# Kernel optimization log

Measured on AMD Instinct MI355X. Metric: run time of the kernel, lower is better.

## Reference

```python
import jax, jax.numpy as jnp
import numpy as np

B, C, VC, H, W = 4, 256, 128, 64, 64


def setup_inputs() -> dict:
    key = jax.random.key(0)
    kx, kq, kk, kv = jax.random.split(key, 4)
    # Conv2d 1x1 no-bias weights are just [out_channels, in_channels] matrices.
    s = 1.0 / np.sqrt(C)
    return {
        "x": jax.random.normal(kx, (B, C, H, W), dtype=jnp.float32),
        "Wq": jax.random.uniform(kq, (VC, C), minval=-s, maxval=s, dtype=jnp.float32),
        "Wk": jax.random.uniform(kk, (VC, C), minval=-s, maxval=s, dtype=jnp.float32),
        "Wv": jax.random.uniform(kv, (VC, C), minval=-s, maxval=s, dtype=jnp.float32),
    }


def reference(x, Wq, Wk, Wv):
    # 1x1 convs == per-pixel channel GEMMs
    Q = jnp.einsum('bchw,dc->bdhw', x, Wq)  # [B, VC, H, W]
    K = jnp.einsum('bchw,dc->bdhw', x, Wk)
    V = jnp.einsum('bchw,dc->bdhw', x, Wv)
    b, d, h, w = Q.shape
    # affinity over all spatial pairs: [B, H, W, H, W]
    aff = jnp.einsum('bdij,bdkl->bijkl', Q, K).reshape(b, h, w, h * w)
    aff = jax.nn.softmax(aff, axis=3).reshape(b, h, w, h, w)
    # attention-weighted aggregation of values
    out = jnp.einsum('bijkl,bdkl->bdij', aff, V)  # [B, VC, H, W]
    return out
```

## Files before the change

kernel.cpp:

```cpp
#include <hip/hip_runtime.h>
#include <hip/hip_bf16.h>

#define B_ 4
#define C_ 256
#define D_ 128
#define N_ 4096

typedef float f32x4 __attribute__((ext_vector_type(4)));
typedef short bf16x8 __attribute__((ext_vector_type(8)));
typedef short s16x4 __attribute__((ext_vector_type(4)));
typedef unsigned short u16;
typedef unsigned int u32;

__device__ __forceinline__ u16 f2bf(float f) {
  unsigned u = __float_as_uint(f);
  u += 0x7fffu + ((u >> 16) & 1u);
  return (u16)(u >> 16);
}
__device__ __forceinline__ float bf2f(u16 v) {
  return __uint_as_float(((u32)v) << 16);
}
__device__ __forceinline__ u32 cvt_pk_bf16(float a, float b) {
  u32 r;
  asm("v_cvt_pk_bf16_f32 %0, %1, %2" : "=v"(r) : "v"(a), "v"(b));
  return r;
}

__global__ __launch_bounds__(256) void castw_kernel(
    const float* __restrict__ Wq, const float* __restrict__ Wk,
    const float* __restrict__ Wv, u16* __restrict__ Whi,
    u16* __restrict__ Wlo) {
  const int i = blockIdx.x * 256 + threadIdx.x;
  const int m = i >> 13;
  const int j = (i & 8191) * 4;
  const float* src = (m == 0) ? Wq : (m == 1) ? Wk : Wv;
  const float scale = (m == 0) ? 1.44269504f : 1.0f;
  const float4 v = *(const float4*)(src + j);
  const float vv[4] = {v.x * scale, v.y * scale, v.z * scale, v.w * scale};
  s16x4 h, l;
#pragma unroll
  for (int k = 0; k < 4; ++k) {
    const u16 hb = f2bf(vv[k]);
    h[k] = (short)hb;
    l[k] = (short)f2bf(vv[k] - bf2f(hb));
  }
  *(s16x4*)&Whi[m * 32768 + j] = h;
  *(s16x4*)&Wlo[m * 32768 + j] = l;
}

__global__ __launch_bounds__(256, 2) void proj_kernel(
    const float* __restrict__ x, const u16* __restrict__ Whi,
    const u16* __restrict__ Wlo, u16* __restrict__ Qo, u16* __restrict__ Ko,
    u16* __restrict__ Vt) {
  __shared__ __align__(16) u16 xs_h[32 * 256];
  __shared__ __align__(16) u16 xs_l[32 * 256];

  const int n0 = blockIdx.x * 32;
  const int b = blockIdx.y;
  const int t = threadIdx.x;
  const int w = t >> 6, lane = t & 63, g = lane >> 4, c = lane & 15;

  {
    const float* xb = x + ((size_t)b * C_) * N_ + n0;
#pragma unroll
    for (int r = 0; r < 8; ++r) {
      const int id = r * 256 + t;
      const int cr = id >> 3, nq = (id & 7) * 4;
      const float4 v = *(const float4*)(xb + (size_t)cr * N_ + nq);
      const float vv[4] = {v.x, v.y, v.z, v.w};
#pragma unroll
      for (int k2 = 0; k2 < 4; ++k2) {
        const int idx2 = (nq + k2) * 256 + (cr ^ (((nq + k2) & 7) << 3));
        const u16 hb = f2bf(vv[k2]);
        xs_h[idx2] = hb;
        xs_l[idx2] = f2bf(vv[k2] - bf2f(hb));
      }
    }
  }
  __syncthreads();

  if (w < 2) {
    const size_t wo = (size_t)w * 32768;
    u16* __restrict__ O = (w == 0 ? Qo : Ko) + (size_t)b * N_ * D_;
#pragma unroll 1
    for (int dt = 0; dt < 8; ++dt) {
      bf16x8 wfh[8], wfl[8];
#pragma unroll
      for (int kc = 0; kc < 8; ++kc) {
        const size_t off = wo + (size_t)(dt * 16 + c) * 256 + kc * 32 + g * 8;
        wfh[kc] = *(const bf16x8*)&Whi[off];
        wfl[kc] = *(const bf16x8*)&Wlo[off];
      }
#pragma unroll
      for (int nt = 0; nt < 2; ++nt) {
        f32x4 a = {0.f, 0.f, 0.f, 0.f};
#pragma unroll
        for (int kc = 0; kc < 8; ++kc) {
          const int xi = (nt * 16 + c) * 256 +
                         ((kc * 32 + g * 8) ^ ((c & 7) << 3));
          const bf16x8 xh = *(const bf16x8*)&xs_h[xi];
          const bf16x8 xl = *(const bf16x8*)&xs_l[xi];
          a = __builtin_amdgcn_mfma_f32_16x16x32_bf16(xh, wfh[kc], a, 0, 0, 0);
          a = __builtin_amdgcn_mfma_f32_16x16x32_bf16(xh, wfl[kc], a, 0, 0, 0);
          a = __builtin_amdgcn_mfma_f32_16x16x32_bf16(xl, wfh[kc], a, 0, 0, 0);
        }
#pragma unroll
        for (int i = 0; i < 4; ++i)
          O[(size_t)(n0 + nt * 16 + g * 4 + i) * D_ + dt * 16 + c] = f2bf(a[i]);
      }
    }
  } else {
    const size_t wo = (size_t)2 * 32768;
    const int d0 = (w - 2) * 64;
    u16* __restrict__ O = Vt + (size_t)b * D_ * N_;
#pragma unroll 1
    for (int dt = 0; dt < 4; ++dt) {
      bf16x8 wfh[8], wfl[8];
#pragma unroll
      for (int kc = 0; kc < 8; ++kc) {
        const size_t off =
            wo + (size_t)(d0 + dt * 16 + c) * 256 + kc * 32 + g * 8;
        wfh[kc] = *(const bf16x8*)&Whi[off];
        wfl[kc] = *(const bf16x8*)&Wlo[off];
      }
#pragma unroll
      for (int nt = 0; nt < 2; ++nt) {
        f32x4 a = {0.f, 0.f, 0.f, 0.f};
#pragma unroll
        for (int kc = 0; kc < 8; ++kc) {
          const int xi = (nt * 16 + c) * 256 +
                         ((kc * 32 + g * 8) ^ ((c & 7) << 3));
          const bf16x8 xh = *(const bf16x8*)&xs_h[xi];
          const bf16x8 xl = *(const bf16x8*)&xs_l[xi];
          a = __builtin_amdgcn_mfma_f32_16x16x32_bf16(wfh[kc], xh, a, 0, 0, 0);
          a = __builtin_amdgcn_mfma_f32_16x16x32_bf16(wfl[kc], xh, a, 0, 0, 0);
          a = __builtin_amdgcn_mfma_f32_16x16x32_bf16(wfh[kc], xl, a, 0, 0, 0);
        }
#pragma unroll
        for (int i = 0; i < 4; ++i)
          O[(size_t)(d0 + dt * 16 + g * 4 + i) * N_ + n0 + nt * 16 + c] =
              f2bf(a[i]);
      }
    }
  }
}

__device__ __forceinline__ int kIdx(int row, int col) {
  return row * 128 + (col ^ ((row & 7) << 3));
}
__device__ __forceinline__ int vIdx(int d, int col) {
  return d * 64 + (col ^ ((d & 7) << 3));
}
__device__ __forceinline__ int kprm(int q) {
  const int ct = q >> 2, qq = q & 3;
  return ((ct >> 1) << 5) +
         (((qq >> 1) == (ct & 1)) ? (qq << 3) : (((qq ^ 2) << 3) + 4));
}

__global__ __launch_bounds__(256, 2) void attn_kernel(
    const u16* __restrict__ Q, const u16* __restrict__ K,
    const u16* __restrict__ Vt, u16* __restrict__ op,
    float* __restrict__ mb, float* __restrict__ lb,
    float* __restrict__ outf, int qt, int rem) {
  __shared__ __align__(16) u16 lds_k[64 * 128];
  __shared__ __align__(16) u16 lds_vt[128 * 64];

  const int b = blockIdx.y;
  const int sid = blockIdx.z;
  const int q0 = blockIdx.x * 128;
  const int NT = qt + (sid < rem ? 1 : 0);
  const int t0 = sid * qt + (sid < rem ? sid : rem);
  const int k0 = t0 * 64;
  const int t = threadIdx.x;
  const int w = t >> 6, lane = t & 63, g = lane >> 4, c = lane & 15;
  const int qw = q0 + w * 32;
  const bool ghi = (g & 2) != 0;

  const u16* __restrict__ Qb = Q + (size_t)b * N_ * D_;
  const u16* __restrict__ Kb = K + (size_t)b * N_ * D_;
  const u16* __restrict__ Vb = Vt + (size_t)b * D_ * N_;

  bf16x8 qf[2][4];
#pragma unroll
  for (int qh = 0; qh < 2; ++qh)
#pragma unroll
    for (int kc = 0; kc < 4; ++kc)
      qf[qh][kc] =
          *(const bf16x8*)&Qb[(size_t)(qw + qh * 16 + c) * D_ + kc * 32 + g * 8];

  f32x4 acc[8][2];
#pragma unroll
  for (int dt = 0; dt < 8; ++dt)
#pragma unroll
    for (int qh = 0; qh < 2; ++qh) acc[dt][qh] = (f32x4){0.f, 0.f, 0.f, 0.f};
  float mrow[2] = {-3.0e38f, -3.0e38f};
  float lrow[2] = {0.f, 0.f};
  const float THR = 11.5415603f;

  bf16x8 krg[4], vrg[4];
  auto load_tile = [&](int kbase) {
#pragma unroll
    for (int i = 0; i < 4; ++i) {
      const int idx = i * 256 + t;
      krg[i] = *(const bf16x8*)&Kb[(size_t)(kbase + (idx >> 4)) * D_ + (idx & 15) * 8];
      vrg[i] = *(const bf16x8*)&Vb[(size_t)(idx >> 3) * N_ + kbase + (idx & 7) * 8];
    }
  };
  load_tile(k0);

  for (int kt = 0; kt < NT; ++kt) {
    __syncthreads();
#pragma unroll
    for (int i = 0; i < 4; ++i) {
      const int idx = i * 256 + t;
      *(bf16x8*)&lds_k[kIdx(idx >> 4, (idx & 15) * 8)] = krg[i];
      const int d = idx >> 3, rc = idx & 7;
      s16x4 lo, hi;
      lo[0] = vrg[i][0]; lo[1] = vrg[i][1]; lo[2] = vrg[i][2]; lo[3] = vrg[i][3];
      hi[0] = vrg[i][4]; hi[1] = vrg[i][5]; hi[2] = vrg[i][6]; hi[3] = vrg[i][7];
      *(s16x4*)&lds_vt[vIdx(d, kprm(rc * 2))] = lo;
      *(s16x4*)&lds_vt[vIdx(d, kprm(rc * 2 + 1))] = hi;
    }
    if (kt + 1 < NT) load_tile(k0 + (kt + 1) * 64);
    __syncthreads();

    f32x4 s[4][2];
#pragma unroll
    for (int ct = 0; ct < 4; ++ct)
#pragma unroll
      for (int qh = 0; qh < 2; ++qh) s[ct][qh] = (f32x4){0.f, 0.f, 0.f, 0.f};
    __builtin_amdgcn_s_setprio(1);
#pragma unroll
    for (int kc = 0; kc < 4; ++kc) {
#pragma unroll
      for (int ct = 0; ct < 4; ++ct) {
        const bf16x8 kf =
            *(const bf16x8*)&lds_k[kIdx(ct * 16 + c, kc * 32 + g * 8)];
        s[ct][0] = __builtin_amdgcn_mfma_f32_16x16x32_bf16(kf, qf[0][kc], s[ct][0], 0, 0, 0);
        s[ct][1] = __builtin_amdgcn_mfma_f32_16x16x32_bf16(kf, qf[1][kc], s[ct][1], 0, 0, 0);
      }
    }
    __builtin_amdgcn_s_setprio(0);

    float pm[2];
#pragma unroll
    for (int qh = 0; qh < 2; ++qh) {
      const float m0 = fmaxf(fmaxf(s[0][qh][0], s[0][qh][1]),
                             fmaxf(s[0][qh][2], s[0][qh][3]));
      const float m1 = fmaxf(fmaxf(s[1][qh][0], s[1][qh][1]),
                             fmaxf(s[1][qh][2], s[1][qh][3]));
      const float m2 = fmaxf(fmaxf(s[2][qh][0], s[2][qh][1]),
                             fmaxf(s[2][qh][2], s[2][qh][3]));
      const float m3 = fmaxf(fmaxf(s[3][qh][0], s[3][qh][1]),
                             fmaxf(s[3][qh][2], s[3][qh][3]));
      float p = fmaxf(fmaxf(m0, m1), fmaxf(m2, m3));
      p = fmaxf(p, __shfl_xor(p, 16));
      p = fmaxf(p, __shfl_xor(p, 32));
      pm[qh] = p;
    }
    const bool need =
        __any((pm[0] > mrow[0] + THR) || (pm[1] > mrow[1] + THR));
    if (need) {
#pragma unroll
      for (int qh = 0; qh < 2; ++qh) {
        const float mnew = fmaxf(mrow[qh], pm[qh]);
        const float scl = exp2f(mrow[qh] - mnew);
        lrow[qh] *= scl;
        mrow[qh] = mnew;
#pragma unroll
        for (int dt = 0; dt < 8; ++dt) {
          acc[dt][qh][0] *= scl; acc[dt][qh][1] *= scl;
          acc[dt][qh][2] *= scl; acc[dt][qh][3] *= scl;
        }
      }
    }
#pragma unroll
    for (int qh = 0; qh < 2; ++qh) {
      float rs = 0.f;
#pragma unroll
      for (int ct = 0; ct < 4; ++ct)
#pragma unroll
        for (int i = 0; i < 4; ++i) {
          const float p = exp2f(s[ct][qh][i] - mrow[qh]);
          s[ct][qh][i] = p;
          rs += p;
        }
      rs += __shfl_xor(rs, 16);
      rs += __shfl_xor(rs, 32);
      lrow[qh] += rs;
    }

    u32 pfw[2][2][4];
#pragma unroll
    for (int kc = 0; kc < 2; ++kc) {
#pragma unroll
      for (int qh = 0; qh < 2; ++qh) {
        const u32 lo0 = cvt_pk_bf16(s[kc * 2][qh][0], s[kc * 2][qh][1]);
        const u32 lo1 = cvt_pk_bf16(s[kc * 2][qh][2], s[kc * 2][qh][3]);
        const u32 hi0 = cvt_pk_bf16(s[kc * 2 + 1][qh][0], s[kc * 2 + 1][qh][1]);
        const u32 hi1 = cvt_pk_bf16(s[kc * 2 + 1][qh][2], s[kc * 2 + 1][qh][3]);
        pfw[kc][qh][0] = ghi ? hi0 : lo0;
        pfw[kc][qh][1] = ghi ? hi1 : lo1;
        const u32 s0 = ghi ? lo0 : hi0;
        const u32 s1 = ghi ? lo1 : hi1;
        pfw[kc][qh][2] = (u32)__shfl_xor((int)s0, 32);
        pfw[kc][qh][3] = (u32)__shfl_xor((int)s1, 32);
      }
    }

#pragma unroll
    for (int kc = 0; kc < 2; ++kc) {
      union { u32 w[4]; bf16x8 v; } u0, u1;
#pragma unroll
      for (int j = 0; j < 4; ++j) { u0.w[j] = pfw[kc][0][j]; u1.w[j] = pfw[kc][1][j]; }
      __builtin_amdgcn_s_setprio(1);
#pragma unroll
      for (int dt = 0; dt < 8; ++dt) {
        const bf16x8 vf =
            *(const bf16x8*)&lds_vt[vIdx(dt * 16 + c, kc * 32 + g * 8)];
        acc[dt][0] = __builtin_amdgcn_mfma_f32_16x16x32_bf16(vf, u0.v, acc[dt][0], 0, 0, 0);
        acc[dt][1] = __builtin_amdgcn_mfma_f32_16x16x32_bf16(vf, u1.v, acc[dt][1], 0, 0, 0);
      }
      __builtin_amdgcn_s_setprio(0);
    }
  }

#pragma unroll
  for (int qh = 0; qh < 2; ++qh) {
    const int n = qw + qh * 16 + c;
    if (mb) {
      u16* __restrict__ ob = op + ((size_t)(sid * B_ + b) * D_) * N_;
#pragma unroll
      for (int dt = 0; dt < 8; ++dt)
#pragma unroll
        for (int i = 0; i < 4; ++i)
          ob[(size_t)(dt * 16 + g * 4 + i) * N_ + n] = f2bf(acc[dt][qh][i]);
      if (g == 0) {
        mb[(size_t)(sid * B_ + b) * N_ + n] = mrow[qh];
        lb[(size_t)(sid * B_ + b) * N_ + n] = lrow[qh];
      }
    } else {
      const float linv = 1.0f / lrow[qh];
      float* __restrict__ ob = outf + (size_t)b * D_ * N_;
#pragma unroll
      for (int dt = 0; dt < 8; ++dt)
#pragma unroll
        for (int i = 0; i < 4; ++i)
          ob[(size_t)(dt * 16 + g * 4 + i) * N_ + n] = acc[dt][qh][i] * linv;
    }
  }
}

__global__ __launch_bounds__(256) void combine_kernel(
    const u16* __restrict__ op, const float* __restrict__ mbu,
    const float* __restrict__ lbu, float* __restrict__ out, int S) {
  const int idx = blockIdx.x * 256 + threadIdx.x;
  const int n0 = (idx & (N_ / 4 - 1)) * 4;
  const int bd = idx >> 10;
  const int b = bd >> 7, d = bd & (D_ - 1);

  float4 msv[8], lsv[8];
  float M0 = -3e38f, M1 = -3e38f, M2 = -3e38f, M3 = -3e38f;
#pragma unroll
  for (int s = 0; s < 8; ++s)
    if (s < S) {
      msv[s] = *(const float4*)&mbu[(size_t)(s * B_ + b) * N_ + n0];
      lsv[s] = *(const float4*)&lbu[(size_t)(s * B_ + b) * N_ + n0];
      M0 = fmaxf(M0, msv[s].x); M1 = fmaxf(M1, msv[s].y);
      M2 = fmaxf(M2, msv[s].z); M3 = fmaxf(M3, msv[s].w);
    }
  float d0 = 0.f, d1 = 0.f, d2 = 0.f, d3 = 0.f;
  float a0 = 0.f, a1 = 0.f, a2 = 0.f, a3 = 0.f;
#pragma unroll
  for (int s = 0; s < 8; ++s)
    if (s < S) {
      const float w0 = exp2f(msv[s].x - M0);
      const float w1 = exp2f(msv[s].y - M1);
      const float w2 = exp2f(msv[s].z - M2);
      const float w3 = exp2f(msv[s].w - M3);
      d0 += lsv[s].x * w0; d1 += lsv[s].y * w1;
      d2 += lsv[s].z * w2; d3 += lsv[s].w * w3;
      const s16x4 o =
          *(const s16x4*)&op[((size_t)(s * B_ + b) * D_ + d) * N_ + n0];
      a0 += w0 * bf2f((u16)o[0]); a1 += w1 * bf2f((u16)o[1]);
      a2 += w2 * bf2f((u16)o[2]); a3 += w3 * bf2f((u16)o[3]);
    }
  float4 r = {a0 / d0, a1 / d1, a2 / d2, a3 / d3};
  *(float4*)&out[((size_t)b * D_ + d) * N_ + n0] = r;
}

extern "C" void kernel_launch(void* const* d_in, const int* in_sizes, int n_in,
                              void* d_out, int out_size, void* d_ws, size_t ws_size,
                              hipStream_t stream) {
  const float* x  = (const float*)d_in[0];
  const float* Wq = (const float*)d_in[1];
  const float* Wk = (const float*)d_in[2];
  const float* Wv = (const float*)d_in[3];
  float* out = (float*)d_out;

  u16* whi  = (u16*)d_ws;
  u16* wlo  = whi + (size_t)3 * 128 * 256;
  u16* q_ws = wlo + (size_t)3 * 128 * 256;
  u16* k_ws = q_ws + (size_t)B_ * N_ * D_;
  u16* v_ws = k_ws + (size_t)B_ * N_ * D_;

  castw_kernel<<<96, 256, 0, stream>>>(Wq, Wk, Wv, whi, wlo);
  proj_kernel<<<dim3(N_ / 32, B_), 256, 0, stream>>>(x, whi, wlo, q_ws, k_ws,
                                                     v_ws);

  const size_t baseB =
      ((size_t)6 * 128 * 256 + (size_t)3 * B_ * N_ * D_) * 2;
  int S = 0;
  const int cands[4] = {6, 4, 2, 1};
  for (int ci = 0; ci < 4; ++ci) {
    const int cand = cands[ci];
    const size_t need = baseB + (size_t)cand * ((size_t)B_ * D_ * N_ * 2 +
                                                (size_t)2 * B_ * N_ * 4);
    if (ws_size >= need) { S = cand; break; }
  }
  if (S > 1) {
    u16* opb = (u16*)((char*)d_ws + baseB);
    float* mbuf = (float*)(opb + (size_t)S * B_ * D_ * N_);
    float* lbuf = mbuf + (size_t)S * B_ * N_;
    attn_kernel<<<dim3(N_ / 128, B_, S), 256, 0, stream>>>(
        q_ws, k_ws, v_ws, opb, mbuf, lbuf, nullptr, 64 / S, 64 % S);
    combine_kernel<<<(B_ * D_ * N_ / 4) / 256, 256, 0, stream>>>(opb, mbuf,
                                                                 lbuf, out, S);
  } else {
    attn_kernel<<<dim3(N_ / 128, B_, 1), 256, 0, stream>>>(
        q_ws, k_ws, v_ws, nullptr, nullptr, nullptr, out, 64, 0);
  }
}
```

Baseline: 103.2 us.

## Compute softmax row sums via MFMA with ones and enlarge projection tiles

The attention kernel no longer reduces softmax row sums with per-lane adds and cross-lane shuffles. It accumulates them with an extra MFMA against a ones vector, using the same bf16-rounded probabilities that feed the PV product. The running-max shuffle reduction now runs only inside the rare rescale branch, and the threshold test uses per-lane partial maxima. The projection kernel moves to 512-thread blocks covering 64 pixels, so each weight-fragment load serves more pixel tiles, at the cost of doubled LDS per block.

```diff
diff --git a/kernel.cpp b/kernel.cpp
--- a/kernel.cpp
+++ b/kernel.cpp
@@ -48,14 +48,14 @@
   *(s16x4*)&Wlo[m * 32768 + j] = l;
 }
 
-__global__ __launch_bounds__(256, 2) void proj_kernel(
+__global__ __launch_bounds__(512, 2) void proj_kernel(
     const float* __restrict__ x, const u16* __restrict__ Whi,
     const u16* __restrict__ Wlo, u16* __restrict__ Qo, u16* __restrict__ Ko,
     u16* __restrict__ Vt) {
-  __shared__ __align__(16) u16 xs_h[32 * 256];
-  __shared__ __align__(16) u16 xs_l[32 * 256];
-
-  const int n0 = blockIdx.x * 32;
+  __shared__ __align__(16) u16 xs_h[64 * 256];
+  __shared__ __align__(16) u16 xs_l[64 * 256];
+
+  const int n0 = blockIdx.x * 64;
   const int b = blockIdx.y;
   const int t = threadIdx.x;
   const int w = t >> 6, lane = t & 63, g = lane >> 4, c = lane & 15;
@@ -64,8 +64,8 @@
     const float* xb = x + ((size_t)b * C_) * N_ + n0;
 #pragma unroll
     for (int r = 0; r < 8; ++r) {
-      const int id = r * 256 + t;
-      const int cr = id >> 3, nq = (id & 7) * 4;
+      const int id = r * 512 + t;
+      const int cr = id >> 4, nq = (id & 15) * 4;
       const float4 v = *(const float4*)(xb + (size_t)cr * N_ + nq);
       const float vv[4] = {v.x, v.y, v.z, v.w};
 #pragma unroll
@@ -79,11 +79,14 @@
   }
   __syncthreads();
 
-  if (w < 2) {
-    const size_t wo = (size_t)w * 32768;
-    u16* __restrict__ O = (w == 0 ? Qo : Ko) + (size_t)b * N_ * D_;
+  if (w < 4) {
+    const int m = w >> 1;
+    const size_t wo = (size_t)m * 32768;
+    const int dtb = (w & 1) * 4;
+    u16* __restrict__ O = (m == 0 ? Qo : Ko) + (size_t)b * N_ * D_;
 #pragma unroll 1
-    for (int dt = 0; dt < 8; ++dt) {
+    for (int dti = 0; dti < 4; ++dti) {
+      const int dt = dtb + dti;
       bf16x8 wfh[8], wfl[8];
 #pragma unroll
       for (int kc = 0; kc < 8; ++kc) {
@@ -92,7 +95,7 @@
         wfl[kc] = *(const bf16x8*)&Wlo[off];
       }
 #pragma unroll
-      for (int nt = 0; nt < 2; ++nt) {
+      for (int nt = 0; nt < 4; ++nt) {
         f32x4 a = {0.f, 0.f, 0.f, 0.f};
 #pragma unroll
         for (int kc = 0; kc < 8; ++kc) {
@@ -111,20 +114,20 @@
     }
   } else {
     const size_t wo = (size_t)2 * 32768;
-    const int d0 = (w - 2) * 64;
+    const int dtb = (w - 4) * 2;
     u16* __restrict__ O = Vt + (size_t)b * D_ * N_;
 #pragma unroll 1
-    for (int dt = 0; dt < 4; ++dt) {
+    for (int dti = 0; dti < 2; ++dti) {
+      const int dt = dtb + dti;
       bf16x8 wfh[8], wfl[8];
 #pragma unroll
       for (int kc = 0; kc < 8; ++kc) {
-        const size_t off =
-            wo + (size_t)(d0 + dt * 16 + c) * 256 + kc * 32 + g * 8;
+        const size_t off = wo + (size_t)(dt * 16 + c) * 256 + kc * 32 + g * 8;
         wfh[kc] = *(const bf16x8*)&Whi[off];
         wfl[kc] = *(const bf16x8*)&Wlo[off];
       }
 #pragma unroll
-      for (int nt = 0; nt < 2; ++nt) {
+      for (int nt = 0; nt < 4; ++nt) {
         f32x4 a = {0.f, 0.f, 0.f, 0.f};
 #pragma unroll
         for (int kc = 0; kc < 8; ++kc) {
@@ -138,8 +141,7 @@
         }
 #pragma unroll
         for (int i = 0; i < 4; ++i)
-          O[(size_t)(d0 + dt * 16 + g * 4 + i) * N_ + n0 + nt * 16 + c] =
-              f2bf(a[i]);
+          O[(size_t)(dt * 16 + g * 4 + i) * N_ + n0 + nt * 16 + c] = f2bf(a[i]);
       }
     }
   }
@@ -189,13 +191,19 @@
           *(const bf16x8*)&Qb[(size_t)(qw + qh * 16 + c) * D_ + kc * 32 + g * 8];
 
   f32x4 acc[8][2];
+  f32x4 accl[2];
 #pragma unroll
   for (int dt = 0; dt < 8; ++dt)
 #pragma unroll
     for (int qh = 0; qh < 2; ++qh) acc[dt][qh] = (f32x4){0.f, 0.f, 0.f, 0.f};
+  accl[0] = (f32x4){0.f, 0.f, 0.f, 0.f};
+  accl[1] = (f32x4){0.f, 0.f, 0.f, 0.f};
   float mrow[2] = {-3.0e38f, -3.0e38f};
-  float lrow[2] = {0.f, 0.f};
   const float THR = 11.5415603f;
+
+  bf16x8 onesv;
+#pragma unroll
+  for (int j = 0; j < 8; ++j) onesv[j] = (short)0x3F80;
 
   bf16x8 krg[4], vrg[4];
   auto load_tile = [&](int kbase) {
@@ -242,7 +250,7 @@
     }
     __builtin_amdgcn_s_setprio(0);
 
-    float pm[2];
+    float pml[2];
 #pragma unroll
     for (int qh = 0; qh < 2; ++qh) {
       const float m0 = fmaxf(fmaxf(s[0][qh][0], s[0][qh][1]),
@@ -253,20 +261,21 @@
                              fmaxf(s[2][qh][2], s[2][qh][3]));
       const float m3 = fmaxf(fmaxf(s[3][qh][0], s[3][qh][1]),
                              fmaxf(s[3][qh][2], s[3][qh][3]));
-      float p = fmaxf(fmaxf(m0, m1), fmaxf(m2, m3));
-      p = fmaxf(p, __shfl_xor(p, 16));
-      p = fmaxf(p, __shfl_xor(p, 32));
-      pm[qh] = p;
+      pml[qh] = fmaxf(fmaxf(m0, m1), fmaxf(m2, m3));
     }
     const bool need =
-        __any((pm[0] > mrow[0] + THR) || (pm[1] > mrow[1] + THR));
+        __any((pml[0] > mrow[0] + THR) || (pml[1] > mrow[1] + THR));
     if (need) {
 #pragma unroll
       for (int qh = 0; qh < 2; ++qh) {
-        const float mnew = fmaxf(mrow[qh], pm[qh]);
+        float p = pml[qh];
+        p = fmaxf(p, __shfl_xor(p, 16));
+        p = fmaxf(p, __shfl_xor(p, 32));
+        const float mnew = fmaxf(mrow[qh], p);
         const float scl = exp2f(mrow[qh] - mnew);
-        lrow[qh] *= scl;
         mrow[qh] = mnew;
+        accl[qh][0] *= scl; accl[qh][1] *= scl;
+        accl[qh][2] *= scl; accl[qh][3] *= scl;
 #pragma unroll
         for (int dt = 0; dt < 8; ++dt) {
           acc[dt][qh][0] *= scl; acc[dt][qh][1] *= scl;
@@ -275,20 +284,12 @@
       }
     }
 #pragma unroll
-    for (int qh = 0; qh < 2; ++qh) {
-      float rs = 0.f;
+    for (int qh = 0; qh < 2; ++qh)
 #pragma unroll
       for (int ct = 0; ct < 4; ++ct)
 #pragma unroll
-        for (int i = 0; i < 4; ++i) {
-          const float p = exp2f(s[ct][qh][i] - mrow[qh]);
-          s[ct][qh][i] = p;
-          rs += p;
-        }
-      rs += __shfl_xor(rs, 16);
-      rs += __shfl_xor(rs, 32);
-      lrow[qh] += rs;
-    }
+        for (int i = 0; i < 4; ++i)
+          s[ct][qh][i] = exp2f(s[ct][qh][i] - mrow[qh]);
 
     u32 pfw[2][2][4];
 #pragma unroll
@@ -314,6 +315,8 @@
 #pragma unroll
       for (int j = 0; j < 4; ++j) { u0.w[j] = pfw[kc][0][j]; u1.w[j] = pfw[kc][1][j]; }
       __builtin_amdgcn_s_setprio(1);
+      accl[0] = __builtin_amdgcn_mfma_f32_16x16x32_bf16(onesv, u0.v, accl[0], 0, 0, 0);
+      accl[1] = __builtin_amdgcn_mfma_f32_16x16x32_bf16(onesv, u1.v, accl[1], 0, 0, 0);
 #pragma unroll
       for (int dt = 0; dt < 8; ++dt) {
         const bf16x8 vf =
@@ -328,6 +331,7 @@
 #pragma unroll
   for (int qh = 0; qh < 2; ++qh) {
     const int n = qw + qh * 16 + c;
+    const float lr = accl[qh][0];
     if (mb) {
       u16* __restrict__ ob = op + ((size_t)(sid * B_ + b) * D_) * N_;
 #pragma unroll
@@ -337,10 +341,10 @@
           ob[(size_t)(dt * 16 + g * 4 + i) * N_ + n] = f2bf(acc[dt][qh][i]);
       if (g == 0) {
         mb[(size_t)(sid * B_ + b) * N_ + n] = mrow[qh];
-        lb[(size_t)(sid * B_ + b) * N_ + n] = lrow[qh];
+        lb[(size_t)(sid * B_ + b) * N_ + n] = lr;
       }
     } else {
-      const float linv = 1.0f / lrow[qh];
+      const float linv = 1.0f / lr;
       float* __restrict__ ob = outf + (size_t)b * D_ * N_;
 #pragma unroll
       for (int dt = 0; dt < 8; ++dt)
@@ -405,7 +409,7 @@
   u16* v_ws = k_ws + (size_t)B_ * N_ * D_;
 
   castw_kernel<<<96, 256, 0, stream>>>(Wq, Wk, Wv, whi, wlo);
-  proj_kernel<<<dim3(N_ / 32, B_), 256, 0, stream>>>(x, whi, wlo, q_ws, k_ws,
+  proj_kernel<<<dim3(N_ / 64, B_), 512, 0, stream>>>(x, whi, wlo, q_ws, k_ws,
                                                      v_ws);
 
   const size_t baseB =
```

Result: no change. 104.9 us (+1.6%).

## Compute softmax row sums via MFMA, defer max shuffles, and remap grid by XCD

Applied to the files above, without the earlier changes.

The per-tile row sum of probabilities is now accumulated by an extra MFMA against a vector of bf16 ones, which removes the VALU adds and cross-lane shuffles for the row sum. The cross-lane max reduction now runs only inside the rarely taken rescale branch, and the trigger check uses per-lane maxima. The launch becomes a 1D grid remapped so that blocks sharing a batch and split land on the same XCD, aiming for better L2 reuse of K/V. The tradeoffs are two extra MFMAs per k-chunk, and a row sum built from bf16-rounded probabilities, which slightly changes numerics.

```diff
diff --git a/kernel.cpp b/kernel.cpp
--- a/kernel.cpp
+++ b/kernel.cpp
@@ -161,13 +161,26 @@
     const u16* __restrict__ Q, const u16* __restrict__ K,
     const u16* __restrict__ Vt, u16* __restrict__ op,
     float* __restrict__ mb, float* __restrict__ lb,
-    float* __restrict__ outf, int qt, int rem) {
+    float* __restrict__ outf, int qt, int rem, int S) {
   __shared__ __align__(16) u16 lds_k[64 * 128];
   __shared__ __align__(16) u16 lds_vt[128 * 64];
 
-  const int b = blockIdx.y;
-  const int sid = blockIdx.z;
-  const int q0 = blockIdx.x * 128;
+  const int L = blockIdx.x;
+  int qx, b, sid;
+  if (((B_ * S) & 7) == 0) {
+    const int gpx = (B_ * S) >> 3;
+    const int xcd = L & 7, idx = L >> 3;
+    const int grp = xcd * gpx + (idx >> 5);
+    qx = idx & 31;
+    b = grp / S;
+    sid = grp - b * S;
+  } else {
+    qx = L & 31;
+    const int r2 = L >> 5;
+    b = r2 % B_;
+    sid = r2 / B_;
+  }
+  const int q0 = qx * 128;
   const int NT = qt + (sid < rem ? 1 : 0);
   const int t0 = sid * qt + (sid < rem ? sid : rem);
   const int k0 = t0 * 64;
@@ -189,13 +202,19 @@
           *(const bf16x8*)&Qb[(size_t)(qw + qh * 16 + c) * D_ + kc * 32 + g * 8];
 
   f32x4 acc[8][2];
+  f32x4 accl[2];
 #pragma unroll
   for (int dt = 0; dt < 8; ++dt)
 #pragma unroll
     for (int qh = 0; qh < 2; ++qh) acc[dt][qh] = (f32x4){0.f, 0.f, 0.f, 0.f};
+  accl[0] = (f32x4){0.f, 0.f, 0.f, 0.f};
+  accl[1] = (f32x4){0.f, 0.f, 0.f, 0.f};
   float mrow[2] = {-3.0e38f, -3.0e38f};
-  float lrow[2] = {0.f, 0.f};
   const float THR = 11.5415603f;
+
+  bf16x8 onesv;
+#pragma unroll
+  for (int j = 0; j < 8; ++j) onesv[j] = (short)0x3F80;
 
   bf16x8 krg[4], vrg[4];
   auto load_tile = [&](int kbase) {
@@ -242,7 +261,7 @@
     }
     __builtin_amdgcn_s_setprio(0);
 
-    float pm[2];
+    float pml[2];
 #pragma unroll
     for (int qh = 0; qh < 2; ++qh) {
       const float m0 = fmaxf(fmaxf(s[0][qh][0], s[0][qh][1]),
@@ -253,20 +272,21 @@
                              fmaxf(s[2][qh][2], s[2][qh][3]));
       const float m3 = fmaxf(fmaxf(s[3][qh][0], s[3][qh][1]),
                              fmaxf(s[3][qh][2], s[3][qh][3]));
-      float p = fmaxf(fmaxf(m0, m1), fmaxf(m2, m3));
-      p = fmaxf(p, __shfl_xor(p, 16));
-      p = fmaxf(p, __shfl_xor(p, 32));
-      pm[qh] = p;
+      pml[qh] = fmaxf(fmaxf(m0, m1), fmaxf(m2, m3));
     }
     const bool need =
-        __any((pm[0] > mrow[0] + THR) || (pm[1] > mrow[1] + THR));
+        __any((pml[0] > mrow[0] + THR) || (pml[1] > mrow[1] + THR));
     if (need) {
 #pragma unroll
       for (int qh = 0; qh < 2; ++qh) {
-        const float mnew = fmaxf(mrow[qh], pm[qh]);
+        float p = pml[qh];
+        p = fmaxf(p, __shfl_xor(p, 16));
+        p = fmaxf(p, __shfl_xor(p, 32));
+        const float mnew = fmaxf(mrow[qh], p);
         const float scl = exp2f(mrow[qh] - mnew);
-        lrow[qh] *= scl;
         mrow[qh] = mnew;
+        accl[qh][0] *= scl; accl[qh][1] *= scl;
+        accl[qh][2] *= scl; accl[qh][3] *= scl;
 #pragma unroll
         for (int dt = 0; dt < 8; ++dt) {
           acc[dt][qh][0] *= scl; acc[dt][qh][1] *= scl;
@@ -275,20 +295,12 @@
       }
     }
 #pragma unroll
-    for (int qh = 0; qh < 2; ++qh) {
-      float rs = 0.f;
+    for (int qh = 0; qh < 2; ++qh)
 #pragma unroll
       for (int ct = 0; ct < 4; ++ct)
 #pragma unroll
-        for (int i = 0; i < 4; ++i) {
-          const float p = exp2f(s[ct][qh][i] - mrow[qh]);
-          s[ct][qh][i] = p;
-          rs += p;
-        }
-      rs += __shfl_xor(rs, 16);
-      rs += __shfl_xor(rs, 32);
-      lrow[qh] += rs;
-    }
+        for (int i = 0; i < 4; ++i)
+          s[ct][qh][i] = exp2f(s[ct][qh][i] - mrow[qh]);
 
     u32 pfw[2][2][4];
 #pragma unroll
@@ -314,6 +326,8 @@
 #pragma unroll
       for (int j = 0; j < 4; ++j) { u0.w[j] = pfw[kc][0][j]; u1.w[j] = pfw[kc][1][j]; }
       __builtin_amdgcn_s_setprio(1);
+      accl[0] = __builtin_amdgcn_mfma_f32_16x16x32_bf16(onesv, u0.v, accl[0], 0, 0, 0);
+      accl[1] = __builtin_amdgcn_mfma_f32_16x16x32_bf16(onesv, u1.v, accl[1], 0, 0, 0);
 #pragma unroll
       for (int dt = 0; dt < 8; ++dt) {
         const bf16x8 vf =
@@ -328,6 +342,7 @@
 #pragma unroll
   for (int qh = 0; qh < 2; ++qh) {
     const int n = qw + qh * 16 + c;
+    const float lr = accl[qh][0];
     if (mb) {
       u16* __restrict__ ob = op + ((size_t)(sid * B_ + b) * D_) * N_;
 #pragma unroll
@@ -337,10 +352,10 @@
           ob[(size_t)(dt * 16 + g * 4 + i) * N_ + n] = f2bf(acc[dt][qh][i]);
       if (g == 0) {
         mb[(size_t)(sid * B_ + b) * N_ + n] = mrow[qh];
-        lb[(size_t)(sid * B_ + b) * N_ + n] = lrow[qh];
+        lb[(size_t)(sid * B_ + b) * N_ + n] = lr;
       }
     } else {
-      const float linv = 1.0f / lrow[qh];
+      const float linv = 1.0f / lr;
       float* __restrict__ ob = outf + (size_t)b * D_ * N_;
 #pragma unroll
       for (int dt = 0; dt < 8; ++dt)
@@ -422,12 +437,12 @@
     u16* opb = (u16*)((char*)d_ws + baseB);
     float* mbuf = (float*)(opb + (size_t)S * B_ * D_ * N_);
     float* lbuf = mbuf + (size_t)S * B_ * N_;
-    attn_kernel<<<dim3(N_ / 128, B_, S), 256, 0, stream>>>(
-        q_ws, k_ws, v_ws, opb, mbuf, lbuf, nullptr, 64 / S, 64 % S);
+    attn_kernel<<<dim3(32 * B_ * S), 256, 0, stream>>>(
+        q_ws, k_ws, v_ws, opb, mbuf, lbuf, nullptr, 64 / S, 64 % S, S);
     combine_kernel<<<(B_ * D_ * N_ / 4) / 256, 256, 0, stream>>>(opb, mbuf,
                                                                  lbuf, out, S);
   } else {
-    attn_kernel<<<dim3(N_ / 128, B_, 1), 256, 0, stream>>>(
-        q_ws, k_ws, v_ws, nullptr, nullptr, nullptr, out, 64, 0);
-  }
-}
+    attn_kernel<<<dim3(32 * B_), 256, 0, stream>>>(
+        q_ws, k_ws, v_ws, nullptr, nullptr, nullptr, out, 64, 0, 1);
+  }
+}
```

Measured after the change: 101.9 us. No clear change (-1.3%).
